# Kernel tuning notes

Hardware: AMD Instinct MI355X
Metric: run time of the kernel (lower is better)

The kernel has to match this reference:

```python
import jax, jax.numpy as jnp
import numpy as np

EPS_THRESH = 1e-10   # threshold used by GraphFilter to sparsify A
NORM_EPS = 1e-12     # torch F.normalize clamp
REG = 2.0 / 3.0      # AGE preprocess_graph reg coefficient (layer=1)


def setup_inputs() -> dict:
    key = jax.random.key(0)
    X = jax.random.normal(key, (8192, 512), dtype=jnp.float32)
    return {"X": X}


def reference(X):
    N = X.shape[0]
    # row L2-normalize (torch F.normalize semantics)
    norms = jnp.maximum(jnp.linalg.norm(X, axis=1, keepdims=True), NORM_EPS)
    feats = X / norms
    # dense cosine-similarity graph, thresholded at epsilon
    A = feats @ feats.T                               # [N, N]
    A = jnp.where(A < EPS_THRESH, 0.0, A)
    # remove self-loops (adj - diag_sparse in the original)
    idx = jnp.arange(N)
    A = A.at[idx, idx].set(0.0)
    # preprocess_graph(norm='sym', renorm=True): adj_ = A + I, sym-normalize
    rowsum = jnp.sum(A, axis=1) + 1.0                 # diag of (A + I)
    d_inv_sqrt = rowsum ** -0.5
    A_norm = A * d_inv_sqrt[:, None] * d_inv_sqrt[None, :]
    # A+I normalized: off-diag from A_norm, diag contributes d_i^-1
    diag_term = d_inv_sqrt * d_inv_sqrt               # = 1/rowsum
    # filter = I - reg * (I - (A_norm + diag(diag_term)))
    #        = (1-reg) I + reg * (A_norm + diag(diag_term))
    # propagate: out = filter @ X
    out = (1.0 - REG) * X + REG * (A_norm @ X + (diag_term[:, None] * X))
    return out
```

## Files before the change

### kernel.cpp

```cpp
#include <hip/hip_runtime.h>


#define NR 8192
#define DC 512
#define KZN 4

typedef unsigned short u16;
typedef signed char i8;
typedef __bf16 bf16x8 __attribute__((ext_vector_type(8)));
typedef float f32x4 __attribute__((ext_vector_type(4)));
typedef int i32x4 __attribute__((ext_vector_type(4)));
typedef u16 u16x8 __attribute__((ext_vector_type(8)));
typedef u16 u16x4 __attribute__((ext_vector_type(4)));

#define QS_INV 254.0f
#define QY_INV 211.6666666f
#define DEQ 1.8600229e-5f

__device__ __forceinline__ float bf2f(u16 u) {
  union { unsigned u; float f; } v; v.u = ((unsigned)u) << 16; return v.f;
}
__device__ __forceinline__ u16 f2bf(float f) {
  union { float f; unsigned u; } v; v.f = f;
  unsigned r = v.u + 0x7fffu + ((v.u >> 16) & 1u);
  return (u16)(r >> 16);
}

__device__ __forceinline__ void async16(const void* ga, void* la) {
  __builtin_amdgcn_global_load_lds(
      (const __attribute__((address_space(1))) unsigned int*)ga,
      (__attribute__((address_space(3))) unsigned int*)la, 16, 0, 0);
}

template <int ROWS>
__device__ __forceinline__ void stage_bf16(const u16* __restrict__ g, int ld,
                                           int row0, int k0, u16* lds,
                                           int wave, int lane) {
  constexpr int PER = (ROWS * 4) / 256;
#pragma unroll
  for (int q = 0; q < PER; ++q) {
    int s = wave * (64 * PER) + q * 64 + lane;
    int r = s >> 2;
    int kq = (s & 3) ^ ((s >> 3) & 3);
    async16(g + (size_t)(row0 + r) * ld + (k0 + kq * 8), lds + s * 8);
  }
}
__device__ __forceinline__ bf16x8 frag_bf16(const u16* lds, int m, int kq) {
  int slot = (m << 2) + (kq ^ ((m >> 1) & 3));
  return *(const bf16x8*)(lds + slot * 8);
}

template <int ROWS>
__device__ __forceinline__ void stage_i8(const i8* __restrict__ g, int ld,
                                         int row0, int k0, i8* lds,
                                         int wave, int lane) {
  constexpr int PER = (ROWS * 4) / 256;
#pragma unroll
  for (int q = 0; q < PER; ++q) {
    int s = wave * (64 * PER) + q * 64 + lane;
    int r = s >> 2;
    int kq = (s & 3) ^ ((s >> 3) & 3);
    async16(g + (size_t)(row0 + r) * ld + (k0 + kq * 16), lds + s * 16);
  }
}
__device__ __forceinline__ i32x4 frag_i8(const i8* lds, int m, int kq) {
  int slot = (m << 2) + (kq ^ ((m >> 1) & 3));
  return *(const i32x4*)(lds + slot * 16);
}

__global__ __launch_bounds__(256) void k_normalize(const float* __restrict__ X,
                                                   u16* __restrict__ F,
                                                   float* __restrict__ rs_partial) {
  int row = blockIdx.x;
  int tid = threadIdx.x;
  if (tid == 0) rs_partial[row] = 0.f;
  const float* xr = X + (size_t)row * DC;
  float v0 = xr[tid];
  float v1 = xr[tid + 256];
  float s = v0 * v0 + v1 * v1;
#pragma unroll
  for (int off = 32; off; off >>= 1) s += __shfl_down(s, off);
  __shared__ float wsum[4];
  if ((tid & 63) == 0) wsum[tid >> 6] = s;
  __syncthreads();
  float tot = wsum[0] + wsum[1] + wsum[2] + wsum[3];
  float scale = 1.0f / fmaxf(sqrtf(tot), 1e-12f);
  u16* fr = F + (size_t)row * DC;
  fr[tid] = f2bf(v0 * scale);
  fr[tid + 256] = f2bf(v1 * scale);
}

__global__ __launch_bounds__(256, 3) void k_simgemm(const u16* __restrict__ F,
                                                    i8* __restrict__ S,
                                                    float* __restrict__ rs_partial) {
  __shared__ alignas(16) char smem[32768];
  u16* As = (u16*)smem;
  u16* Bs = (u16*)(smem + 8192);
  int tid = threadIdx.x, lane = tid & 63, wave = tid >> 6;
  int b = blockIdx.x;
  int tj = (int)((sqrtf(8.f * b + 1.f) - 1.f) * 0.5f);
  while ((tj + 1) * (tj + 2) / 2 <= b) ++tj;
  while (tj * (tj + 1) / 2 > b) --tj;
  int ti = b - tj * (tj + 1) / 2;
  bool diag = (ti == tj);

  int wm = wave >> 1, wn = wave & 1;
  int quad = lane >> 4, col = lane & 15;
  f32x4 zero = {0.f, 0.f, 0.f, 0.f};
  f32x4 acc[4][4];
#pragma unroll
  for (int a = 0; a < 4; ++a)
#pragma unroll
    for (int c = 0; c < 4; ++c) acc[a][c] = zero;

  const u16* Bsrc = diag ? As : Bs;
  for (int kt = 0; kt < DC; kt += 32) {
    __syncthreads();
    stage_bf16<128>(F, DC, ti * 128, kt, As, wave, lane);
    if (!diag) stage_bf16<128>(F, DC, tj * 128, kt, Bs, wave, lane);
    __syncthreads();
    bf16x8 af[4], bfr[4];
#pragma unroll
    for (int mi = 0; mi < 4; ++mi) af[mi] = frag_bf16(As, wm * 64 + mi * 16 + col, quad);
#pragma unroll
    for (int ni = 0; ni < 4; ++ni) bfr[ni] = frag_bf16(Bsrc, wn * 64 + ni * 16 + col, quad);
#pragma unroll
    for (int mi = 0; mi < 4; ++mi)
#pragma unroll
      for (int ni = 0; ni < 4; ++ni)
        acc[mi][ni] = __builtin_amdgcn_mfma_f32_16x16x32_bf16(af[mi], bfr[ni], acc[mi][ni], 0, 0, 0);
  }

  float cs[4] = {0.f, 0.f, 0.f, 0.f};
  float rv[16];
#pragma unroll
  for (int u = 0; u < 16; ++u) rv[u] = 0.f;
#pragma unroll
  for (int mi = 0; mi < 4; ++mi) {
#pragma unroll
    for (int r = 0; r < 4; ++r) {
      int gi = ti * 128 + wm * 64 + mi * 16 + quad * 4 + r;
#pragma unroll
      for (int ni = 0; ni < 4; ++ni) {
        int gj = tj * 128 + wn * 64 + ni * 16 + col;
        float v = acc[mi][ni][r];
        if (v < 1e-10f || gi == gj) v = 0.f;
        acc[mi][ni][r] = v;
        cs[ni] += v;
        rv[mi * 4 + r] += v;
      }
    }
  }
#pragma unroll
  for (int ni = 0; ni < 4; ++ni) {
    float c = cs[ni];
    c += __shfl_xor(c, 16);
    c += __shfl_xor(c, 32);
    if (quad == 0) {
      int gj = tj * 128 + wn * 64 + ni * 16 + col;
      atomicAdd(&rs_partial[gj], c);
    }
  }
  if (!diag) {
#pragma unroll
    for (int u = 0; u < 16; ++u) {
      float c = rv[u];
      c += __shfl_xor(c, 1);
      c += __shfl_xor(c, 2);
      c += __shfl_xor(c, 4);
      c += __shfl_xor(c, 8);
      if (col == 0) {
        int mi = u >> 2, r = u & 3;
        int gi = ti * 128 + wm * 64 + mi * 16 + quad * 4 + r;
        atomicAdd(&rs_partial[gi], c);
      }
    }
  }

  char* direct = smem;
  char* mirror = smem + 16384;
  __syncthreads();
#pragma unroll
  for (int mi = 0; mi < 4; ++mi) {
#pragma unroll
    for (int ni = 0; ni < 4; ++ni) {
      int cg = wn * 64 + ni * 16 + col;
      int q[4];
#pragma unroll
      for (int r = 0; r < 4; ++r) {
        int qq = (int)rintf(acc[mi][ni][r] * QS_INV);
        q[r] = qq > 127 ? 127 : qq;
      }
#pragma unroll
      for (int r = 0; r < 4; ++r) {
        int row = wm * 64 + mi * 16 + quad * 4 + r;
        int chunk = (cg >> 4) ^ (row & 7);
        direct[row * 128 + chunk * 16 + (cg & 15)] = (char)q[r];
      }
      if (!diag) {
        int mcb = wm * 64 + mi * 16 + quad * 4;
        int chunk = (mcb >> 4) ^ (cg & 7);
        unsigned pk = (unsigned)(q[0] & 255) | ((unsigned)(q[1] & 255) << 8) |
                      ((unsigned)(q[2] & 255) << 16) | ((unsigned)(q[3] & 255) << 24);
        *(unsigned*)(mirror + cg * 128 + chunk * 16 + (mcb & 15)) = pk;
      }
    }
  }
  __syncthreads();
  {
    int r2 = tid >> 1, half = tid & 1;
#pragma unroll
    for (int k = 0; k < 4; ++k) {
      int c = half * 4 + k;
      int phys = c ^ (r2 & 7);
      i32x4 d = *(const i32x4*)(direct + r2 * 128 + phys * 16);
      *(i32x4*)(S + (size_t)(ti * 128 + r2) * NR + tj * 128 + c * 16) = d;
    }
    if (!diag) {
#pragma unroll
      for (int k = 0; k < 4; ++k) {
        int c = half * 4 + k;
        int phys = c ^ (r2 & 7);
        i32x4 d = *(const i32x4*)(mirror + r2 * 128 + phys * 16);
        *(i32x4*)(S + (size_t)(tj * 128 + r2) * NR + ti * 128 + c * 16) = d;
      }
    }
  }
}

__global__ __launch_bounds__(256) void k_dinv(const float* __restrict__ rs_partial,
                                              float* __restrict__ dinv,
                                              float* __restrict__ invrow) {
  int i = blockIdx.x * 256 + threadIdx.x;
  float rs = rs_partial[i] + 1.0f;
  dinv[i] = 1.0f / sqrtf(rs);
  invrow[i] = 1.0f / rs;
}

__global__ __launch_bounds__(256) void k_make_yt(const float* __restrict__ X,
                                                 const float* __restrict__ dinv,
                                                 i8* __restrict__ Yt) {
  __shared__ float T[64][65];
  int i0 = blockIdx.x * 64, k0 = blockIdx.y * 64;
  int tid = threadIdx.x;
  {
    int iL = tid >> 2, ks = (tid & 3) * 4;
    const float* xr = X + (size_t)(i0 + iL) * DC + k0;
#pragma unroll
    for (int u = 0; u < 4; ++u) {
      float4 f = *(const float4*)(xr + ks + u * 16);
      T[iL][ks + u * 16 + 0] = f.x;
      T[iL][ks + u * 16 + 1] = f.y;
      T[iL][ks + u * 16 + 2] = f.z;
      T[iL][ks + u * 16 + 3] = f.w;
    }
  }
  __syncthreads();
  {
    int kL = tid >> 2, ib = (tid & 3) * 16;
    char pk[16];
#pragma unroll
    for (int u = 0; u < 16; ++u) {
      float v = T[ib + u][kL] * dinv[i0 + ib + u];
      int q = (int)rintf(v * QY_INV);
      q = q > 127 ? 127 : (q < -127 ? -127 : q);
      pk[u] = (char)q;
    }
    *(i32x4*)(Yt + (size_t)(k0 + kL) * NR + i0 + ib) = *(const i32x4*)pk;
  }
}

__global__ __launch_bounds__(256, 2) void k_outgemm(const i8* __restrict__ S,
                                                    const i8* __restrict__ Yt,
                                                    u16* __restrict__ Pb) {
  __shared__ alignas(16) i8 As[128 * 64];
  __shared__ alignas(16) i8 Bs[256 * 64];
  int tid = threadIdx.x, lane = tid & 63, wave = tid >> 6;
  int tn = blockIdx.x, ti = blockIdx.y, kz = blockIdx.z;
  int wm = wave & 1, wn = wave >> 1;
  int quad = lane >> 4, col = lane & 15;
  i32x4 zero = {0, 0, 0, 0};
  i32x4 acc[4][8];
#pragma unroll
  for (int a = 0; a < 4; ++a)
#pragma unroll
    for (int c = 0; c < 8; ++c) acc[a][c] = zero;

  const int KCH = NR / KZN;
  int k_lo = kz * KCH, k_hi = k_lo + KCH;
  for (int kt = k_lo; kt < k_hi; kt += 64) {
    __syncthreads();
    stage_i8<128>(S, NR, ti * 128, kt, As, wave, lane);
    stage_i8<256>(Yt, NR, tn * 256, kt, Bs, wave, lane);
    __syncthreads();
    i32x4 af[4], bfr[8];
#pragma unroll
    for (int mi = 0; mi < 4; ++mi) af[mi] = frag_i8(As, wm * 64 + mi * 16 + col, quad);
#pragma unroll
    for (int ni = 0; ni < 8; ++ni) bfr[ni] = frag_i8(Bs, wn * 128 + ni * 16 + col, quad);
#pragma unroll
    for (int mi = 0; mi < 4; ++mi)
#pragma unroll
      for (int ni = 0; ni < 8; ++ni)
        acc[mi][ni] = __builtin_amdgcn_mfma_i32_16x16x64_i8(af[mi], bfr[ni], acc[mi][ni], 0, 0, 0);
  }
#pragma unroll
  for (int mi = 0; mi < 4; ++mi) {
#pragma unroll
    for (int r = 0; r < 4; ++r) {
      int gi = ti * 128 + wm * 64 + mi * 16 + quad * 4 + r;
#pragma unroll
      for (int ni = 0; ni < 8; ++ni) {
        int gj = tn * 256 + wn * 128 + ni * 16 + col;
        Pb[((size_t)kz * NR + gi) * DC + gj] = f2bf((float)acc[mi][ni][r] * DEQ);
      }
    }
  }
}

__global__ __launch_bounds__(256) void k_reduce(const u16* __restrict__ Pb,
                                               const float* __restrict__ X,
                                               const float* __restrict__ dinv,
                                               const float* __restrict__ invrow,
                                               float* __restrict__ out) {
  const float c1 = (float)(2.0 / 3.0);
  const float c0 = 1.0f - c1;
  size_t idx = ((size_t)blockIdx.x * 256 + threadIdx.x) * 4;
  int i = (int)(idx >> 9);
  float4 s = {0.f, 0.f, 0.f, 0.f};
#pragma unroll
  for (int kz = 0; kz < KZN; ++kz) {
    u16x4 p = *(const u16x4*)(Pb + (size_t)kz * NR * DC + idx);
    s.x += bf2f(p[0]); s.y += bf2f(p[1]); s.z += bf2f(p[2]); s.w += bf2f(p[3]);
  }
  float4 x = *(const float4*)(X + idx);
  float sc = c1 * dinv[i];
  float xs = c0 + c1 * invrow[i];
  float4 o = {xs * x.x + sc * s.x, xs * x.y + sc * s.y,
              xs * x.z + sc * s.z, xs * x.w + sc * s.w};
  *(float4*)(out + idx) = o;
}

extern "C" void kernel_launch(void* const* d_in, const int* in_sizes, int n_in,
                              void* d_out, int out_size, void* d_ws, size_t ws_size,
                              hipStream_t stream) {
  const float* X = (const float*)d_in[0];
  float* out = (float*)d_out;
  char* ws = (char*)d_ws;
  i8*  S  = (i8*)(ws);
  u16* F  = (u16*)(ws + 67108864);
  i8*  Yt = (i8*)(ws + 75497472);
  float* rs_partial = (float*)(ws + 79691776);
  float* dinv       = (float*)(ws + 79724544);
  float* invrow     = (float*)(ws + 79757312);
  u16* Pb = (u16*)(ws + 79790080);

  k_normalize<<<dim3(NR), dim3(256), 0, stream>>>(X, F, rs_partial);
  k_simgemm<<<dim3(64 * 65 / 2), dim3(256), 0, stream>>>(F, S, rs_partial);
  k_dinv<<<dim3(NR / 256), dim3(256), 0, stream>>>(rs_partial, dinv, invrow);
  k_make_yt<<<dim3(128, 8), dim3(256), 0, stream>>>(X, dinv, Yt);
  k_outgemm<<<dim3(2, 64, KZN), dim3(256), 0, stream>>>(S, Yt, Pb);
  k_reduce<<<dim3(NR * DC / 1024), dim3(256), 0, stream>>>(Pb, X, dinv, invrow, out);
}
```

Before: 203.6 us.

## Deepen simgemm K-step, widen outgemm to 8 waves, double split-K

The similarity GEMM now stages two 32-wide K slices per barrier pair, with separate A and B buffers for each slice. This halves the number of synchronisations, and the launch-bounds occupancy hint rises to 4. The int8 output GEMM now runs 512 threads per block, so each wave holds a 64x64 accumulator tile instead of 64x128, which cuts register pressure. Split-K rises from 4 to 8 chunks to expose more blocks. The cost is twice the bf16 partial-sum buffer, which must be written and then re-read by the reduce kernel, and that larger buffer may not fit in the workspace.

```diff
diff --git a/kernel.cpp b/kernel.cpp
--- a/kernel.cpp
+++ b/kernel.cpp
@@ -3,7 +3,7 @@
 
 #define NR 8192
 #define DC 512
-#define KZN 4
+#define KZN 8
 
 typedef unsigned short u16;
 typedef signed char i8;
@@ -32,14 +32,12 @@
       (__attribute__((address_space(3))) unsigned int*)la, 16, 0, 0);
 }
 
-template <int ROWS>
-__device__ __forceinline__ void stage_bf16(const u16* __restrict__ g, int ld,
-                                           int row0, int k0, u16* lds,
-                                           int wave, int lane) {
-  constexpr int PER = (ROWS * 4) / 256;
-#pragma unroll
-  for (int q = 0; q < PER; ++q) {
-    int s = wave * (64 * PER) + q * 64 + lane;
+__device__ __forceinline__ void stage_bf16_128(const u16* __restrict__ g, int ld,
+                                               int row0, int k0, u16* lds,
+                                               int wave, int lane) {
+#pragma unroll
+  for (int q = 0; q < 2; ++q) {
+    int s = wave * 128 + q * 64 + lane;
     int r = s >> 2;
     int kq = (s & 3) ^ ((s >> 3) & 3);
     async16(g + (size_t)(row0 + r) * ld + (k0 + kq * 8), lds + s * 8);
@@ -50,14 +48,13 @@
   return *(const bf16x8*)(lds + slot * 8);
 }
 
-template <int ROWS>
+template <int ROWS, int NT>
 __device__ __forceinline__ void stage_i8(const i8* __restrict__ g, int ld,
-                                         int row0, int k0, i8* lds,
-                                         int wave, int lane) {
-  constexpr int PER = (ROWS * 4) / 256;
+                                         int row0, int k0, i8* lds, int tid) {
+  constexpr int PER = (ROWS * 4) / NT;
 #pragma unroll
   for (int q = 0; q < PER; ++q) {
-    int s = wave * (64 * PER) + q * 64 + lane;
+    int s = q * NT + tid;
     int r = s >> 2;
     int kq = (s & 3) ^ ((s >> 3) & 3);
     async16(g + (size_t)(row0 + r) * ld + (k0 + kq * 16), lds + s * 16);
@@ -90,12 +87,14 @@
   fr[tid + 256] = f2bf(v1 * scale);
 }
 
-__global__ __launch_bounds__(256, 3) void k_simgemm(const u16* __restrict__ F,
+__global__ __launch_bounds__(256, 4) void k_simgemm(const u16* __restrict__ F,
                                                     i8* __restrict__ S,
                                                     float* __restrict__ rs_partial) {
   __shared__ alignas(16) char smem[32768];
-  u16* As = (u16*)smem;
-  u16* Bs = (u16*)(smem + 8192);
+  u16* As  = (u16*)smem;
+  u16* As2 = (u16*)(smem + 8192);
+  u16* Bs  = (u16*)(smem + 16384);
+  u16* Bs2 = (u16*)(smem + 24576);
   int tid = threadIdx.x, lane = tid & 63, wave = tid >> 6;
   int b = blockIdx.x;
   int tj = (int)((sqrtf(8.f * b + 1.f) - 1.f) * 0.5f);
@@ -113,22 +112,30 @@
 #pragma unroll
     for (int c = 0; c < 4; ++c) acc[a][c] = zero;
 
-  const u16* Bsrc = diag ? As : Bs;
-  for (int kt = 0; kt < DC; kt += 32) {
+  for (int kt = 0; kt < DC; kt += 64) {
     __syncthreads();
-    stage_bf16<128>(F, DC, ti * 128, kt, As, wave, lane);
-    if (!diag) stage_bf16<128>(F, DC, tj * 128, kt, Bs, wave, lane);
+    stage_bf16_128(F, DC, ti * 128, kt, As, wave, lane);
+    stage_bf16_128(F, DC, ti * 128, kt + 32, As2, wave, lane);
+    if (!diag) {
+      stage_bf16_128(F, DC, tj * 128, kt, Bs, wave, lane);
+      stage_bf16_128(F, DC, tj * 128, kt + 32, Bs2, wave, lane);
+    }
     __syncthreads();
-    bf16x8 af[4], bfr[4];
-#pragma unroll
-    for (int mi = 0; mi < 4; ++mi) af[mi] = frag_bf16(As, wm * 64 + mi * 16 + col, quad);
-#pragma unroll
-    for (int ni = 0; ni < 4; ++ni) bfr[ni] = frag_bf16(Bsrc, wn * 64 + ni * 16 + col, quad);
-#pragma unroll
-    for (int mi = 0; mi < 4; ++mi)
-#pragma unroll
-      for (int ni = 0; ni < 4; ++ni)
-        acc[mi][ni] = __builtin_amdgcn_mfma_f32_16x16x32_bf16(af[mi], bfr[ni], acc[mi][ni], 0, 0, 0);
+#pragma unroll
+    for (int kk = 0; kk < 2; ++kk) {
+      const u16* Ak = kk ? As2 : As;
+      const u16* Bk = diag ? Ak : (kk ? Bs2 : Bs);
+      bf16x8 af[4], bfr[4];
+#pragma unroll
+      for (int mi = 0; mi < 4; ++mi) af[mi] = frag_bf16(Ak, wm * 64 + mi * 16 + col, quad);
+#pragma unroll
+      for (int ni = 0; ni < 4; ++ni) bfr[ni] = frag_bf16(Bk, wn * 64 + ni * 16 + col, quad);
+#pragma unroll
+      for (int mi = 0; mi < 4; ++mi)
+#pragma unroll
+        for (int ni = 0; ni < 4; ++ni)
+          acc[mi][ni] = __builtin_amdgcn_mfma_f32_16x16x32_bf16(af[mi], bfr[ni], acc[mi][ni], 0, 0, 0);
+    }
   }
 
   float cs[4] = {0.f, 0.f, 0.f, 0.f};
@@ -270,7 +277,7 @@
   }
 }
 
-__global__ __launch_bounds__(256, 2) void k_outgemm(const i8* __restrict__ S,
+__global__ __launch_bounds__(512, 4) void k_outgemm(const i8* __restrict__ S,
                                                     const i8* __restrict__ Yt,
                                                     u16* __restrict__ Pb) {
   __shared__ alignas(16) i8 As[128 * 64];
@@ -280,28 +287,28 @@
   int wm = wave & 1, wn = wave >> 1;
   int quad = lane >> 4, col = lane & 15;
   i32x4 zero = {0, 0, 0, 0};
-  i32x4 acc[4][8];
+  i32x4 acc[4][4];
 #pragma unroll
   for (int a = 0; a < 4; ++a)
 #pragma unroll
-    for (int c = 0; c < 8; ++c) acc[a][c] = zero;
+    for (int c = 0; c < 4; ++c) acc[a][c] = zero;
 
   const int KCH = NR / KZN;
   int k_lo = kz * KCH, k_hi = k_lo + KCH;
   for (int kt = k_lo; kt < k_hi; kt += 64) {
     __syncthreads();
-    stage_i8<128>(S, NR, ti * 128, kt, As, wave, lane);
-    stage_i8<256>(Yt, NR, tn * 256, kt, Bs, wave, lane);
+    stage_i8<128, 512>(S, NR, ti * 128, kt, As, tid);
+    stage_i8<256, 512>(Yt, NR, tn * 256, kt, Bs, tid);
     __syncthreads();
-    i32x4 af[4], bfr[8];
+    i32x4 af[4], bfr[4];
 #pragma unroll
     for (int mi = 0; mi < 4; ++mi) af[mi] = frag_i8(As, wm * 64 + mi * 16 + col, quad);
 #pragma unroll
-    for (int ni = 0; ni < 8; ++ni) bfr[ni] = frag_i8(Bs, wn * 128 + ni * 16 + col, quad);
+    for (int ni = 0; ni < 4; ++ni) bfr[ni] = frag_i8(Bs, wn * 64 + ni * 16 + col, quad);
 #pragma unroll
     for (int mi = 0; mi < 4; ++mi)
 #pragma unroll
-      for (int ni = 0; ni < 8; ++ni)
+      for (int ni = 0; ni < 4; ++ni)
         acc[mi][ni] = __builtin_amdgcn_mfma_i32_16x16x64_i8(af[mi], bfr[ni], acc[mi][ni], 0, 0, 0);
   }
 #pragma unroll
@@ -310,8 +317,8 @@
     for (int r = 0; r < 4; ++r) {
       int gi = ti * 128 + wm * 64 + mi * 16 + quad * 4 + r;
 #pragma unroll
-      for (int ni = 0; ni < 8; ++ni) {
-        int gj = tn * 256 + wn * 128 + ni * 16 + col;
+      for (int ni = 0; ni < 4; ++ni) {
+        int gj = tn * 256 + wn * 64 + ni * 16 + col;
         Pb[((size_t)kz * NR + gi) * DC + gj] = f2bf((float)acc[mi][ni][r] * DEQ);
       }
     }
@@ -359,6 +366,6 @@
   k_simgemm<<<dim3(64 * 65 / 2), dim3(256), 0, stream>>>(F, S, rs_partial);
   k_dinv<<<dim3(NR / 256), dim3(256), 0, stream>>>(rs_partial, dinv, invrow);
   k_make_yt<<<dim3(128, 8), dim3(256), 0, stream>>>(X, dinv, Yt);
-  k_outgemm<<<dim3(2, 64, KZN), dim3(256), 0, stream>>>(S, Yt, Pb);
+  k_outgemm<<<dim3(2, 64, KZN), dim3(512), 0, stream>>>(S, Yt, Pb);
   k_reduce<<<dim3(NR * DC / 1024), dim3(256), 0, stream>>>(Pb, X, dinv, invrow, out);
 }
```

Measured after the change: 207.3 us. About the same (+1.8%).
